# Kernel optimization log

Measured on AMD Instinct MI355X. Metric: run time of the kernel, lower is better.

Reference implementation:

```python
import jax, jax.numpy as jnp
import numpy as np

B, S, H, NH = 4, 2048, 1024, 16
HD = H // NH  # head dim 64


def setup_inputs() -> dict:
    key = jax.random.key(0)
    ks = jax.random.split(key, 8)
    s = 1.0 / np.sqrt(H)
    return {
        "hidden_states": jax.random.normal(ks[0], (B, S, H), dtype=jnp.float32),
        "attention_mask": jnp.zeros((B, 1, 1, S), dtype=jnp.float32),
        "Wq": jax.random.normal(ks[1], (H, H), dtype=jnp.float32) * s,
        "bq": jnp.zeros((H,), dtype=jnp.float32),
        "Wk": jax.random.normal(ks[2], (H, H), dtype=jnp.float32) * s,
        "bk": jnp.zeros((H,), dtype=jnp.float32),
        "Wv": jax.random.normal(ks[3], (H, H), dtype=jnp.float32) * s,
        "bv": jnp.zeros((H,), dtype=jnp.float32),
    }


def _split_heads(x):
    # [B,S,H] -> [B,NH,S,HD]
    b, s, _ = x.shape
    return x.reshape(b, s, NH, HD).transpose(0, 2, 1, 3)


def reference(hidden_states, attention_mask, Wq, bq, Wk, bk, Wv, bv):
    q = _split_heads(hidden_states @ Wq.T + bq)
    k = _split_heads(hidden_states @ Wk.T + bk)
    v = _split_heads(hidden_states @ Wv.T + bv)

    qk = jnp.einsum("bhid,bhjd->bhij", q, k)  # [B,NH,S,S]
    seq = q.shape[2]
    causal = jnp.triu(jnp.ones((seq, seq), dtype=bool), 1)  # True above diagonal
    attn_w = jnp.where(causal, -jnp.inf, qk) + attention_mask
    # NOTE: original divides by sqrt(d_k) AFTER masking/adding attention_mask
    probs = jax.nn.softmax(attn_w / jnp.sqrt(jnp.float32(HD)), axis=-1)
    out = jnp.einsum("bhij,bhjd->bhid", probs, v)  # [B,NH,S,HD]
    return out.transpose(0, 2, 1, 3).reshape(hidden_states.shape[0], seq, NH * HD)
```

## Files before the change

kernel.cpp:

```cpp
#include <hip/hip_runtime.h>


#define B_   4
#define S_   2048
#define H_   1024
#define NH_  16
#define HD_  64
#define M_   (B_ * S_)

#define CEXP 0.18033688011112042f

#define SWZ(row, col) ((col) ^ (((row) & 7) << 3))

typedef float          f32x4  __attribute__((ext_vector_type(4)));
typedef short          bf16x8 __attribute__((ext_vector_type(8)));
typedef unsigned short u16x8  __attribute__((ext_vector_type(8)));

__device__ __forceinline__ unsigned short f2bf(float f) {
    unsigned int u = __float_as_uint(f);
    u += 0x7fffu + ((u >> 16) & 1u);
    return (unsigned short)(u >> 16);
}

__device__ __forceinline__ void load16_lds(const unsigned short* g, unsigned short* l) {
    __builtin_amdgcn_global_load_lds(
        (const __attribute__((address_space(1))) unsigned int*)g,
        (__attribute__((address_space(3))) unsigned int*)l, 16, 0, 0);
}

__global__ __launch_bounds__(256) void cast_bf16(
    const float* __restrict__ s0, const float* __restrict__ s1,
    const float* __restrict__ s2, const float* __restrict__ s3,
    const float* __restrict__ s4,
    unsigned short* __restrict__ d0, unsigned short* __restrict__ d1,
    unsigned short* __restrict__ d2, unsigned short* __restrict__ d3,
    float* __restrict__ d4) {
    const int z = blockIdx.y;
    int i = (blockIdx.x * 256 + threadIdx.x) * 8;
    if (z == 4) {
        if (i + 8 <= B_ * S_) {
            float4 a = *(const float4*)(s4 + i);
            float4 b = *(const float4*)(s4 + i + 4);
            a.x *= CEXP; a.y *= CEXP; a.z *= CEXP; a.w *= CEXP;
            b.x *= CEXP; b.y *= CEXP; b.z *= CEXP; b.w *= CEXP;
            *(float4*)(d4 + i)     = a;
            *(float4*)(d4 + i + 4) = b;
        }
        return;
    }
    const float* src = (z == 0) ? s0 : (z == 1) ? s1 : (z == 2) ? s2 : s3;
    unsigned short* dst = (z == 0) ? d0 : (z == 1) ? d1 : (z == 2) ? d2 : d3;
    const int n = (z == 0) ? M_ * H_ : H_ * H_;
    if (i + 8 <= n) {
        float4 a = *(const float4*)(src + i);
        float4 b = *(const float4*)(src + i + 4);
        u16x8 o;
        o[0] = f2bf(a.x); o[1] = f2bf(a.y); o[2] = f2bf(a.z); o[3] = f2bf(a.w);
        o[4] = f2bf(b.x); o[5] = f2bf(b.y); o[6] = f2bf(b.z); o[7] = f2bf(b.w);
        *(u16x8*)(dst + i) = o;
    }
}

__global__ __launch_bounds__(256, 3) void qkv_gemm(
    const unsigned short* __restrict__ A,
    const unsigned short* __restrict__ W0, const unsigned short* __restrict__ W1,
    const unsigned short* __restrict__ W2,
    const float* __restrict__ b0, const float* __restrict__ b1,
    const float* __restrict__ b2,
    unsigned short* __restrict__ o0, unsigned short* __restrict__ o1,
    unsigned short* __restrict__ o2) {
    __shared__ unsigned short smem[2 * 128 * 64];
    unsigned short* sA = smem;
    unsigned short* sB = smem + 128 * 64;
    unsigned short* sT = smem;

    const int t = threadIdx.x;
    const int w = t >> 6, lane = t & 63, quad = lane >> 4, l15 = lane & 15;
    const int bm = blockIdx.x, bn = blockIdx.y, z = blockIdx.z;

    const unsigned short* W = (z == 0) ? W0 : (z == 1) ? W1 : W2;
    const float*        bia = (z == 0) ? b0 : (z == 1) ? b1 : b2;

    const int wm = (w & 1) * 64, wn = (w >> 1) * 64;

    f32x4 acc[4][4];
#pragma unroll
    for (int i = 0; i < 4; ++i)
#pragma unroll
        for (int j = 0; j < 4; ++j) acc[i][j] = f32x4{0.f, 0.f, 0.f, 0.f};

    const int srow = w * 32 + (lane >> 3);
    const int scol = (lane & 7) * 8;
    const unsigned short* Ag = A + (size_t)(bm * 128 + srow) * H_ + scol;
    const unsigned short* Wg = W + (size_t)(bn * 128 + srow) * H_ + scol;
    unsigned short* lA = &sA[w * 32 * 64];
    unsigned short* lB = &sB[w * 32 * 64];

    for (int kt = 0; kt < 16; ++kt) {
        __syncthreads();
#pragma unroll
        for (int c = 0; c < 4; ++c) {
            load16_lds(Ag + kt * 64 + (size_t)c * 8 * H_, lA + c * 512);
            load16_lds(Wg + kt * 64 + (size_t)c * 8 * H_, lB + c * 512);
        }
        __syncthreads();
#pragma unroll
        for (int kk = 0; kk < 64; kk += 32) {
            bf16x8 af[4], bf[4];
#pragma unroll
            for (int mi = 0; mi < 4; ++mi)
                af[mi] = *(const bf16x8*)&sA[(wm + mi * 16 + l15) * 64 + kk + quad * 8];
#pragma unroll
            for (int ni = 0; ni < 4; ++ni)
                bf[ni] = *(const bf16x8*)&sB[(wn + ni * 16 + l15) * 64 + kk + quad * 8];
#pragma unroll
            for (int mi = 0; mi < 4; ++mi)
#pragma unroll
                for (int ni = 0; ni < 4; ++ni)
                    acc[mi][ni] = __builtin_amdgcn_mfma_f32_16x16x32_bf16(
                        af[mi], bf[ni], acc[mi][ni], 0, 0, 0);
        }
    }

    float bvv[4];
#pragma unroll
    for (int ni = 0; ni < 4; ++ni) bvv[ni] = bia[bn * 128 + wn + ni * 16 + l15];

    if (z != 2) {
        unsigned short* outp = (z == 0) ? o0 : o1;
#pragma unroll
        for (int mi = 0; mi < 4; ++mi)
#pragma unroll
            for (int ni = 0; ni < 4; ++ni)
#pragma unroll
                for (int r = 0; r < 4; ++r) {
                    int m = bm * 128 + wm + mi * 16 + quad * 4 + r;
                    int n = bn * 128 + wn + ni * 16 + l15;
                    outp[(size_t)m * H_ + n] = f2bf(acc[mi][ni][r] + bvv[ni]);
                }
    } else {
        __syncthreads();
        const int halfw = w >> 1;
        const int bb = bm >> 4;
        const int s0 = (bm * 128) & 2047;
        for (int half = 0; half < 2; ++half) {
            if (half) __syncthreads();
            if (halfw == half) {
#pragma unroll
                for (int mi = 0; mi < 4; ++mi)
#pragma unroll
                    for (int ni = 0; ni < 4; ++ni)
#pragma unroll
                        for (int r = 0; r < 4; ++r) {
                            int nl = ni * 16 + l15;
                            int m  = wm + mi * 16 + quad * 4 + r;
                            sT[nl * 136 + m] = f2bf(acc[mi][ni][r] + bvv[ni]);
                        }
            }
            __syncthreads();
            {
                int nl = t >> 2, mc = (t & 3) * 32;
                int ng = bn * 128 + half * 64 + nl;
                int hh = ng >> 6, d = ng & 63;
                size_t base = ((size_t)((bb * NH_ + hh) * HD_ + d)) * S_ + s0 + mc;
#pragma unroll
                for (int i = 0; i < 4; ++i)
                    *(u16x8*)(o2 + base + i * 8) = *(const u16x8*)&sT[nl * 136 + mc + i * 8];
            }
        }
    }
}

__global__ __launch_bounds__(256, 3) void attn(
    const unsigned short* __restrict__ qg, const unsigned short* __restrict__ kg,
    const unsigned short* __restrict__ vtg, const float* __restrict__ mcg,
    float* __restrict__ outg) {
    __shared__ unsigned short k_s[2][64 * 64];
    __shared__ unsigned short v_s[2][64 * 64];
    __shared__ unsigned short p_s[4][16 * 64];

    const int t = threadIdx.x;
    const int w = t >> 6, lane = t & 63, quad = lane >> 4, l15 = lane & 15;
    const int lid = blockIdx.x;
    const int bh = (lid & 7) + ((lid >> 7) << 3);
    const int qt = (lid >> 3) & 15;
    const int b = bh >> 4, h = bh & 15;
    const int qa = qt, qb = 31 - qt;

    const int rs_ = t >> 2;
    const int cs_ = (t & 3) * 16;
    const int sc0 = rs_ * 64 + SWZ(rs_, cs_);
    const int sc1 = rs_ * 64 + SWZ(rs_, cs_ + 8);

    const unsigned short* kbase = kg + ((size_t)b * S_ + rs_) * H_ + h * HD_ + cs_;
    const unsigned short* vbase = vtg + ((size_t)bh * HD_ + rs_) * S_ + cs_;
    const float* mbase = mcg + b * S_ + l15;

    bf16x8 aqa[2], aqb[2];
    {
        const unsigned short* qpa =
            qg + ((size_t)(b * S_ + qa * 64 + w * 16 + l15)) * H_ + h * HD_ + quad * 8;
        aqa[0] = *(const bf16x8*)qpa;
        aqa[1] = *(const bf16x8*)(qpa + 32);
        const unsigned short* qpb =
            qg + ((size_t)(b * S_ + qb * 64 + w * 16 + l15)) * H_ + h * HD_ + quad * 8;
        aqb[0] = *(const bf16x8*)qpb;
        aqb[1] = *(const bf16x8*)(qpb + 32);
    }

    u16x8 pk0 = *(const u16x8*)kbase, pk1 = *(const u16x8*)(kbase + 8);
    u16x8 pv0 = *(const u16x8*)vbase, pv1 = *(const u16x8*)(vbase + 8);
    float pmc[4];
#pragma unroll
    for (int j = 0; j < 4; ++j) pmc[j] = mbase[j * 16];

    f32x4 oa[4], ob[4];
    float la[4] = {0.f, 0.f, 0.f, 0.f}, lb[4] = {0.f, 0.f, 0.f, 0.f};
#pragma unroll
    for (int dt = 0; dt < 4; ++dt) {
        oa[dt] = f32x4{0.f, 0.f, 0.f, 0.f};
        ob[dt] = f32x4{0.f, 0.f, 0.f, 0.f};
    }

    const int iga0 = qa * 64 + w * 16 + quad * 4;
    const int igb0 = qb * 64 + w * 16 + quad * 4;

    for (int kt = 0; kt <= qb; ++kt) {
        const int cur = kt & 1;
        *(u16x8*)&k_s[cur][sc0] = pk0;
        *(u16x8*)&k_s[cur][sc1] = pk1;
        *(u16x8*)&v_s[cur][sc0] = pv0;
        *(u16x8*)&v_s[cur][sc1] = pv1;
        float mc_[4];
#pragma unroll
        for (int j = 0; j < 4; ++j) mc_[j] = pmc[j];
        if (kt < qb) {
            const unsigned short* kp = kbase + (size_t)(kt + 1) * 64 * H_;
            pk0 = *(const u16x8*)kp; pk1 = *(const u16x8*)(kp + 8);
            const unsigned short* vp = vbase + (kt + 1) * 64;
            pv0 = *(const u16x8*)vp; pv1 = *(const u16x8*)(vp + 8);
#pragma unroll
            for (int j = 0; j < 4; ++j) pmc[j] = mbase[(kt + 1) * 64 + j * 16];
        }
        __syncthreads();

        {
            f32x4 sc[4];
#pragma unroll
            for (int jt = 0; jt < 4; ++jt) sc[jt] = f32x4{0.f, 0.f, 0.f, 0.f};
            __builtin_amdgcn_s_setprio(1);
#pragma unroll
            for (int c = 0; c < 2; ++c)
#pragma unroll
                for (int jt = 0; jt < 4; ++jt) {
                    int row = jt * 16 + l15;
                    bf16x8 bk = *(const bf16x8*)&k_s[cur][row * 64 + SWZ(row, c * 32 + quad * 8)];
                    sc[jt] = __builtin_amdgcn_mfma_f32_16x16x32_bf16(aqb[c], bk, sc[jt], 0, 0, 0);
                }
            __builtin_amdgcn_s_setprio(0);
            const bool diag = (kt == qb);
#pragma unroll
            for (int r = 0; r < 4; ++r) {
                float ls = 0.f;
                const int prow = quad * 4 + r;
#pragma unroll
                for (int jt = 0; jt < 4; ++jt) {
                    float p = __builtin_amdgcn_exp2f(__builtin_fmaf(sc[jt][r], CEXP, mc_[jt]));
                    if (diag && (kt * 64 + jt * 16 + l15) > (igb0 + r)) p = 0.f;
                    ls += p;
                    unsigned int u = __float_as_uint(p) + 0x8000u;
                    p_s[w][prow * 64 + SWZ(prow, jt * 16 + l15)] = (unsigned short)(u >> 16);
                }
                lb[r] += ls;
            }
            __builtin_amdgcn_s_setprio(1);
#pragma unroll
            for (int c = 0; c < 2; ++c) {
                bf16x8 ap = *(const bf16x8*)&p_s[w][l15 * 64 + SWZ(l15, c * 32 + quad * 8)];
#pragma unroll
                for (int dt = 0; dt < 4; ++dt) {
                    int row = dt * 16 + l15;
                    bf16x8 bv = *(const bf16x8*)&v_s[cur][row * 64 + SWZ(row, c * 32 + quad * 8)];
                    ob[dt] = __builtin_amdgcn_mfma_f32_16x16x32_bf16(ap, bv, ob[dt], 0, 0, 0);
                }
            }
            __builtin_amdgcn_s_setprio(0);
        }
        if (kt <= qa) {
            f32x4 sc[4];
#pragma unroll
            for (int jt = 0; jt < 4; ++jt) sc[jt] = f32x4{0.f, 0.f, 0.f, 0.f};
            __builtin_amdgcn_s_setprio(1);
#pragma unroll
            for (int c = 0; c < 2; ++c)
#pragma unroll
                for (int jt = 0; jt < 4; ++jt) {
                    int row = jt * 16 + l15;
                    bf16x8 bk = *(const bf16x8*)&k_s[cur][row * 64 + SWZ(row, c * 32 + quad * 8)];
                    sc[jt] = __builtin_amdgcn_mfma_f32_16x16x32_bf16(aqa[c], bk, sc[jt], 0, 0, 0);
                }
            __builtin_amdgcn_s_setprio(0);
            const bool diag = (kt == qa);
#pragma unroll
            for (int r = 0; r < 4; ++r) {
                float ls = 0.f;
                const int prow = quad * 4 + r;
#pragma unroll
                for (int jt = 0; jt < 4; ++jt) {
                    float p = __builtin_amdgcn_exp2f(__builtin_fmaf(sc[jt][r], CEXP, mc_[jt]));
                    if (diag && (kt * 64 + jt * 16 + l15) > (iga0 + r)) p = 0.f;
                    ls += p;
                    unsigned int u = __float_as_uint(p) + 0x8000u;
                    p_s[w][prow * 64 + SWZ(prow, jt * 16 + l15)] = (unsigned short)(u >> 16);
                }
                la[r] += ls;
            }
            __builtin_amdgcn_s_setprio(1);
#pragma unroll
            for (int c = 0; c < 2; ++c) {
                bf16x8 ap = *(const bf16x8*)&p_s[w][l15 * 64 + SWZ(l15, c * 32 + quad * 8)];
#pragma unroll
                for (int dt = 0; dt < 4; ++dt) {
                    int row = dt * 16 + l15;
                    bf16x8 bv = *(const bf16x8*)&v_s[cur][row * 64 + SWZ(row, c * 32 + quad * 8)];
                    oa[dt] = __builtin_amdgcn_mfma_f32_16x16x32_bf16(ap, bv, oa[dt], 0, 0, 0);
                }
            }
            __builtin_amdgcn_s_setprio(0);
        }
    }

#pragma unroll
    for (int r = 0; r < 4; ++r) {
        float sa = la[r], sb = lb[r];
#pragma unroll
        for (int mk = 1; mk <= 8; mk <<= 1) {
            sa += __shfl_xor(sa, mk);
            sb += __shfl_xor(sb, mk);
        }
        la[r] = 1.0f / sa;
        lb[r] = 1.0f / sb;
    }
#pragma unroll
    for (int dt = 0; dt < 4; ++dt)
#pragma unroll
        for (int r = 0; r < 4; ++r) {
            int col = h * HD_ + dt * 16 + l15;
            outg[(size_t)(b * S_ + iga0 + r) * H_ + col] = oa[dt][r] * la[r];
            outg[(size_t)(b * S_ + igb0 + r) * H_ + col] = ob[dt][r] * lb[r];
        }
}

extern "C" void kernel_launch(void* const* d_in, const int* in_sizes, int n_in,
                              void* d_out, int out_size, void* d_ws, size_t ws_size,
                              hipStream_t stream) {
    const float* hs   = (const float*)d_in[0];
    const float* mask = (const float*)d_in[1];
    const float* Wq   = (const float*)d_in[2];
    const float* bq   = (const float*)d_in[3];
    const float* Wk   = (const float*)d_in[4];
    const float* bk   = (const float*)d_in[5];
    const float* Wv   = (const float*)d_in[6];
    const float* bv   = (const float*)d_in[7];
    float* out = (float*)d_out;

    unsigned short* hsb = (unsigned short*)d_ws;
    unsigned short* wqb = hsb + (size_t)M_ * H_;
    unsigned short* wkb = wqb + (size_t)H_ * H_;
    unsigned short* wvb = wkb + (size_t)H_ * H_;
    unsigned short* qb  = wvb + (size_t)H_ * H_;
    unsigned short* kb  = qb  + (size_t)M_ * H_;
    unsigned short* vtb = kb  + (size_t)M_ * H_;
    float*          mcw = (float*)(vtb + (size_t)M_ * H_);

    cast_bf16<<<dim3((M_ * H_) / 2048, 5), 256, 0, stream>>>(
        hs, Wq, Wk, Wv, mask, hsb, wqb, wkb, wvb, mcw);

    qkv_gemm<<<dim3(M_ / 128, H_ / 128, 3), 256, 0, stream>>>(
        hsb, wqb, wkb, wvb, bq, bk, bv, qb, kb, vtb);

    attn<<<dim3(1024), 256, 0, stream>>>(qb, kb, vtb, mcw, out);
}
```

Baseline: 235.1 us.

## Interleave both query tiles' QK and PV MFMAs to share K/V fragment loads

Both query tiles (qa and qb) now run their QK^T MFMAs unconditionally in one loop that shares each K fragment read from LDS. Each tile writes its probabilities to its own LDS buffer, and the PV MFMAs are likewise interleaved so every V fragment is read once for both tiles. This halves K/V LDS reads and gives the MFMA pipe two independent accumulation chains to overlap. The cost is wasted MFMA work for tile qa on iterations past its causal range (it multiplies zeroed probabilities), extra LDS for the second P buffer, and higher register pressure that may hurt occupancy at 3 blocks per SM.

```diff
diff --git a/kernel.cpp b/kernel.cpp
--- a/kernel.cpp
+++ b/kernel.cpp
@@ -177,7 +177,8 @@
     float* __restrict__ outg) {
     __shared__ unsigned short k_s[2][64 * 64];
     __shared__ unsigned short v_s[2][64 * 64];
-    __shared__ unsigned short p_s[4][16 * 64];
+    __shared__ unsigned short pa_s[4][16 * 64];
+    __shared__ unsigned short pb_s[4][16 * 64];
 
     const int t = threadIdx.x;
     const int w = t >> 6, lane = t & 63, quad = lane >> 4, l15 = lane & 15;
@@ -244,20 +245,27 @@
         }
         __syncthreads();
 
+        const bool runa = (kt <= qa);
+
+        f32x4 sca[4], scb[4];
+#pragma unroll
+        for (int jt = 0; jt < 4; ++jt) {
+            sca[jt] = f32x4{0.f, 0.f, 0.f, 0.f};
+            scb[jt] = f32x4{0.f, 0.f, 0.f, 0.f};
+        }
+        __builtin_amdgcn_s_setprio(1);
+#pragma unroll
+        for (int c = 0; c < 2; ++c)
+#pragma unroll
+            for (int jt = 0; jt < 4; ++jt) {
+                int row = jt * 16 + l15;
+                bf16x8 bk = *(const bf16x8*)&k_s[cur][row * 64 + SWZ(row, c * 32 + quad * 8)];
+                scb[jt] = __builtin_amdgcn_mfma_f32_16x16x32_bf16(aqb[c], bk, scb[jt], 0, 0, 0);
+                sca[jt] = __builtin_amdgcn_mfma_f32_16x16x32_bf16(aqa[c], bk, sca[jt], 0, 0, 0);
+            }
+        __builtin_amdgcn_s_setprio(0);
+
         {
-            f32x4 sc[4];
-#pragma unroll
-            for (int jt = 0; jt < 4; ++jt) sc[jt] = f32x4{0.f, 0.f, 0.f, 0.f};
-            __builtin_amdgcn_s_setprio(1);
-#pragma unroll
-            for (int c = 0; c < 2; ++c)
-#pragma unroll
-                for (int jt = 0; jt < 4; ++jt) {
-                    int row = jt * 16 + l15;
-                    bf16x8 bk = *(const bf16x8*)&k_s[cur][row * 64 + SWZ(row, c * 32 + quad * 8)];
-                    sc[jt] = __builtin_amdgcn_mfma_f32_16x16x32_bf16(aqb[c], bk, sc[jt], 0, 0, 0);
-                }
-            __builtin_amdgcn_s_setprio(0);
             const bool diag = (kt == qb);
 #pragma unroll
             for (int r = 0; r < 4; ++r) {
@@ -265,41 +273,16 @@
                 const int prow = quad * 4 + r;
 #pragma unroll
                 for (int jt = 0; jt < 4; ++jt) {
-                    float p = __builtin_amdgcn_exp2f(__builtin_fmaf(sc[jt][r], CEXP, mc_[jt]));
+                    float p = __builtin_amdgcn_exp2f(__builtin_fmaf(scb[jt][r], CEXP, mc_[jt]));
                     if (diag && (kt * 64 + jt * 16 + l15) > (igb0 + r)) p = 0.f;
                     ls += p;
                     unsigned int u = __float_as_uint(p) + 0x8000u;
-                    p_s[w][prow * 64 + SWZ(prow, jt * 16 + l15)] = (unsigned short)(u >> 16);
+                    pb_s[w][prow * 64 + SWZ(prow, jt * 16 + l15)] = (unsigned short)(u >> 16);
                 }
                 lb[r] += ls;
             }
-            __builtin_amdgcn_s_setprio(1);
-#pragma unroll
-            for (int c = 0; c < 2; ++c) {
-                bf16x8 ap = *(const bf16x8*)&p_s[w][l15 * 64 + SWZ(l15, c * 32 + quad * 8)];
-#pragma unroll
-                for (int dt = 0; dt < 4; ++dt) {
-                    int row = dt * 16 + l15;
-                    bf16x8 bv = *(const bf16x8*)&v_s[cur][row * 64 + SWZ(row, c * 32 + quad * 8)];
-                    ob[dt] = __builtin_amdgcn_mfma_f32_16x16x32_bf16(ap, bv, ob[dt], 0, 0, 0);
-                }
-            }
-            __builtin_amdgcn_s_setprio(0);
-        }
-        if (kt <= qa) {
-            f32x4 sc[4];
-#pragma unroll
-            for (int jt = 0; jt < 4; ++jt) sc[jt] = f32x4{0.f, 0.f, 0.f, 0.f};
-            __builtin_amdgcn_s_setprio(1);
-#pragma unroll
-            for (int c = 0; c < 2; ++c)
-#pragma unroll
-                for (int jt = 0; jt < 4; ++jt) {
-                    int row = jt * 16 + l15;
-                    bf16x8 bk = *(const bf16x8*)&k_s[cur][row * 64 + SWZ(row, c * 32 + quad * 8)];
-                    sc[jt] = __builtin_amdgcn_mfma_f32_16x16x32_bf16(aqa[c], bk, sc[jt], 0, 0, 0);
-                }
-            __builtin_amdgcn_s_setprio(0);
+        }
+        if (runa) {
             const bool diag = (kt == qa);
 #pragma unroll
             for (int r = 0; r < 4; ++r) {
@@ -307,27 +290,31 @@
                 const int prow = quad * 4 + r;
 #pragma unroll
                 for (int jt = 0; jt < 4; ++jt) {
-                    float p = __builtin_amdgcn_exp2f(__builtin_fmaf(sc[jt][r], CEXP, mc_[jt]));
+                    float p = __builtin_amdgcn_exp2f(__builtin_fmaf(sca[jt][r], CEXP, mc_[jt]));
                     if (diag && (kt * 64 + jt * 16 + l15) > (iga0 + r)) p = 0.f;
                     ls += p;
                     unsigned int u = __float_as_uint(p) + 0x8000u;
-                    p_s[w][prow * 64 + SWZ(prow, jt * 16 + l15)] = (unsigned short)(u >> 16);
+                    pa_s[w][prow * 64 + SWZ(prow, jt * 16 + l15)] = (unsigned short)(u >> 16);
                 }
                 la[r] += ls;
             }
-            __builtin_amdgcn_s_setprio(1);
-#pragma unroll
-            for (int c = 0; c < 2; ++c) {
-                bf16x8 ap = *(const bf16x8*)&p_s[w][l15 * 64 + SWZ(l15, c * 32 + quad * 8)];
-#pragma unroll
-                for (int dt = 0; dt < 4; ++dt) {
-                    int row = dt * 16 + l15;
-                    bf16x8 bv = *(const bf16x8*)&v_s[cur][row * 64 + SWZ(row, c * 32 + quad * 8)];
-                    oa[dt] = __builtin_amdgcn_mfma_f32_16x16x32_bf16(ap, bv, oa[dt], 0, 0, 0);
-                }
-            }
-            __builtin_amdgcn_s_setprio(0);
-        }
+        }
+
+        __builtin_amdgcn_s_setprio(1);
+#pragma unroll
+        for (int c = 0; c < 2; ++c) {
+            bf16x8 apb = *(const bf16x8*)&pb_s[w][l15 * 64 + SWZ(l15, c * 32 + quad * 8)];
+            bf16x8 apa = *(const bf16x8*)&pa_s[w][l15 * 64 + SWZ(l15, c * 32 + quad * 8)];
+            if (!runa) apa = bf16x8{0, 0, 0, 0, 0, 0, 0, 0};
+#pragma unroll
+            for (int dt = 0; dt < 4; ++dt) {
+                int row = dt * 16 + l15;
+                bf16x8 bv = *(const bf16x8*)&v_s[cur][row * 64 + SWZ(row, c * 32 + quad * 8)];
+                ob[dt] = __builtin_amdgcn_mfma_f32_16x16x32_bf16(apb, bv, ob[dt], 0, 0, 0);
+                oa[dt] = __builtin_amdgcn_mfma_f32_16x16x32_bf16(apa, bv, oa[dt], 0, 0, 0);
+            }
+        }
+        __builtin_amdgcn_s_setprio(0);
     }
 
 #pragma unroll
```

Result: slower. 251.1 us (+6.8%).

## Transpose QK MFMA operands, pack softmax probs with cvt_pk_bf16, compact cast grid

Applied to the files above, without the earlier changes.

The attention kernel swaps the QK^T MFMA operands so each lane holds four consecutive key columns for one query row. That lets it read the mask as float4 vectors, convert pairs of probabilities with v_cvt_pk_bf16_f32, and write 8-byte packed stores to LDS instead of scalar 16-bit stores. The row-sum reduction becomes a per-lane scalar plus two cross-quad shuffles, redistributed at the end. The cast kernel is flattened into a 1D grid sized exactly to the work, which removes idle blocks from the old 5x4096 grid; the mask loads now happen after the barrier instead of being prefetched.

```diff
diff --git a/kernel.cpp b/kernel.cpp
--- a/kernel.cpp
+++ b/kernel.cpp
@@ -15,11 +15,18 @@
 typedef float          f32x4  __attribute__((ext_vector_type(4)));
 typedef short          bf16x8 __attribute__((ext_vector_type(8)));
 typedef unsigned short u16x8  __attribute__((ext_vector_type(8)));
+typedef unsigned int   u32x2  __attribute__((ext_vector_type(2)));
 
 __device__ __forceinline__ unsigned short f2bf(float f) {
     unsigned int u = __float_as_uint(f);
     u += 0x7fffu + ((u >> 16) & 1u);
     return (unsigned short)(u >> 16);
+}
+
+__device__ __forceinline__ unsigned int cvt_pk_bf16(float lo, float hi) {
+    unsigned int r;
+    asm("v_cvt_pk_bf16_f32 %0, %1, %2" : "=v"(r) : "v"(lo), "v"(hi));
+    return r;
 }
 
 __device__ __forceinline__ void load16_lds(const unsigned short* g, unsigned short* l) {
@@ -35,9 +42,9 @@
     unsigned short* __restrict__ d0, unsigned short* __restrict__ d1,
     unsigned short* __restrict__ d2, unsigned short* __restrict__ d3,
     float* __restrict__ d4) {
-    const int z = blockIdx.y;
-    int i = (blockIdx.x * 256 + threadIdx.x) * 8;
-    if (z == 4) {
+    const int bid = blockIdx.x;
+    if (bid >= 5632) {
+        int i = ((bid - 5632) * 256 + (int)threadIdx.x) * 8;
         if (i + 8 <= B_ * S_) {
             float4 a = *(const float4*)(s4 + i);
             float4 b = *(const float4*)(s4 + i + 4);
@@ -48,17 +55,20 @@
         }
         return;
     }
-    const float* src = (z == 0) ? s0 : (z == 1) ? s1 : (z == 2) ? s2 : s3;
-    unsigned short* dst = (z == 0) ? d0 : (z == 1) ? d1 : (z == 2) ? d2 : d3;
-    const int n = (z == 0) ? M_ * H_ : H_ * H_;
-    if (i + 8 <= n) {
-        float4 a = *(const float4*)(src + i);
-        float4 b = *(const float4*)(src + i + 4);
-        u16x8 o;
-        o[0] = f2bf(a.x); o[1] = f2bf(a.y); o[2] = f2bf(a.z); o[3] = f2bf(a.w);
-        o[4] = f2bf(b.x); o[5] = f2bf(b.y); o[6] = f2bf(b.z); o[7] = f2bf(b.w);
-        *(u16x8*)(dst + i) = o;
-    }
+    const float* src;
+    unsigned short* dst;
+    int base;
+    if (bid < 4096)      { src = s0; dst = d0; base = bid; }
+    else if (bid < 4608) { src = s1; dst = d1; base = bid - 4096; }
+    else if (bid < 5120) { src = s2; dst = d2; base = bid - 4608; }
+    else                 { src = s3; dst = d3; base = bid - 5120; }
+    int i = (base * 256 + (int)threadIdx.x) * 8;
+    float4 a = *(const float4*)(src + i);
+    float4 b = *(const float4*)(src + i + 4);
+    u16x8 o;
+    o[0] = f2bf(a.x); o[1] = f2bf(a.y); o[2] = f2bf(a.z); o[3] = f2bf(a.w);
+    o[4] = f2bf(b.x); o[5] = f2bf(b.y); o[6] = f2bf(b.z); o[7] = f2bf(b.w);
+    *(u16x8*)(dst + i) = o;
 }
 
 __global__ __launch_bounds__(256, 3) void qkv_gemm(
@@ -194,7 +204,7 @@
 
     const unsigned short* kbase = kg + ((size_t)b * S_ + rs_) * H_ + h * HD_ + cs_;
     const unsigned short* vbase = vtg + ((size_t)bh * HD_ + rs_) * S_ + cs_;
-    const float* mbase = mcg + b * S_ + l15;
+    const float* mrow = mcg + b * S_ + quad * 4;
 
     bf16x8 aqa[2], aqb[2];
     {
@@ -210,20 +220,20 @@
 
     u16x8 pk0 = *(const u16x8*)kbase, pk1 = *(const u16x8*)(kbase + 8);
     u16x8 pv0 = *(const u16x8*)vbase, pv1 = *(const u16x8*)(vbase + 8);
-    float pmc[4];
-#pragma unroll
-    for (int j = 0; j < 4; ++j) pmc[j] = mbase[j * 16];
 
     f32x4 oa[4], ob[4];
-    float la[4] = {0.f, 0.f, 0.f, 0.f}, lb[4] = {0.f, 0.f, 0.f, 0.f};
+    float lsa = 0.f, lsb = 0.f;
 #pragma unroll
     for (int dt = 0; dt < 4; ++dt) {
         oa[dt] = f32x4{0.f, 0.f, 0.f, 0.f};
         ob[dt] = f32x4{0.f, 0.f, 0.f, 0.f};
     }
 
-    const int iga0 = qa * 64 + w * 16 + quad * 4;
-    const int igb0 = qb * 64 + w * 16 + quad * 4;
+    const int iga0  = qa * 64 + w * 16 + quad * 4;
+    const int igb0  = qb * 64 + w * 16 + quad * 4;
+    const int qcola = qa * 64 + w * 16 + l15;
+    const int qcolb = qb * 64 + w * 16 + l15;
+    const int pwr0 = l15 * 64;
 
     for (int kt = 0; kt <= qb; ++kt) {
         const int cur = kt & 1;
@@ -231,18 +241,18 @@
         *(u16x8*)&k_s[cur][sc1] = pk1;
         *(u16x8*)&v_s[cur][sc0] = pv0;
         *(u16x8*)&v_s[cur][sc1] = pv1;
-        float mc_[4];
-#pragma unroll
-        for (int j = 0; j < 4; ++j) mc_[j] = pmc[j];
         if (kt < qb) {
             const unsigned short* kp = kbase + (size_t)(kt + 1) * 64 * H_;
             pk0 = *(const u16x8*)kp; pk1 = *(const u16x8*)(kp + 8);
             const unsigned short* vp = vbase + (kt + 1) * 64;
             pv0 = *(const u16x8*)vp; pv1 = *(const u16x8*)(vp + 8);
-#pragma unroll
-            for (int j = 0; j < 4; ++j) pmc[j] = mbase[(kt + 1) * 64 + j * 16];
         }
         __syncthreads();
+
+        float4 mcv[4];
+#pragma unroll
+        for (int jt = 0; jt < 4; ++jt)
+            mcv[jt] = *(const float4*)(mrow + kt * 64 + jt * 16);
 
         {
             f32x4 sc[4];
@@ -255,23 +265,28 @@
                 for (int jt = 0; jt < 4; ++jt) {
                     int row = jt * 16 + l15;
                     bf16x8 bk = *(const bf16x8*)&k_s[cur][row * 64 + SWZ(row, c * 32 + quad * 8)];
-                    sc[jt] = __builtin_amdgcn_mfma_f32_16x16x32_bf16(aqb[c], bk, sc[jt], 0, 0, 0);
+                    sc[jt] = __builtin_amdgcn_mfma_f32_16x16x32_bf16(bk, aqb[c], sc[jt], 0, 0, 0);
                 }
             __builtin_amdgcn_s_setprio(0);
             const bool diag = (kt == qb);
 #pragma unroll
-            for (int r = 0; r < 4; ++r) {
-                float ls = 0.f;
-                const int prow = quad * 4 + r;
-#pragma unroll
-                for (int jt = 0; jt < 4; ++jt) {
-                    float p = __builtin_amdgcn_exp2f(__builtin_fmaf(sc[jt][r], CEXP, mc_[jt]));
-                    if (diag && (kt * 64 + jt * 16 + l15) > (igb0 + r)) p = 0.f;
-                    ls += p;
-                    unsigned int u = __float_as_uint(p) + 0x8000u;
-                    p_s[w][prow * 64 + SWZ(prow, jt * 16 + l15)] = (unsigned short)(u >> 16);
-                }
-                lb[r] += ls;
+            for (int jt = 0; jt < 4; ++jt) {
+                const int sb0 = kt * 64 + jt * 16 + quad * 4;
+                float p0 = __builtin_amdgcn_exp2f(__builtin_fmaf(sc[jt][0], CEXP, mcv[jt].x));
+                float p1 = __builtin_amdgcn_exp2f(__builtin_fmaf(sc[jt][1], CEXP, mcv[jt].y));
+                float p2 = __builtin_amdgcn_exp2f(__builtin_fmaf(sc[jt][2], CEXP, mcv[jt].z));
+                float p3 = __builtin_amdgcn_exp2f(__builtin_fmaf(sc[jt][3], CEXP, mcv[jt].w));
+                if (diag) {
+                    if (sb0 + 0 > qcolb) p0 = 0.f;
+                    if (sb0 + 1 > qcolb) p1 = 0.f;
+                    if (sb0 + 2 > qcolb) p2 = 0.f;
+                    if (sb0 + 3 > qcolb) p3 = 0.f;
+                }
+                lsb += (p0 + p1) + (p2 + p3);
+                u32x2 pw;
+                pw[0] = cvt_pk_bf16(p0, p1);
+                pw[1] = cvt_pk_bf16(p2, p3);
+                *(u32x2*)&p_s[w][pwr0 + SWZ(l15, jt * 16 + quad * 4)] = pw;
             }
             __builtin_amdgcn_s_setprio(1);
 #pragma unroll
@@ -297,23 +312,28 @@
                 for (int jt = 0; jt < 4; ++jt) {
                     int row = jt * 16 + l15;
                     bf16x8 bk = *(const bf16x8*)&k_s[cur][row * 64 + SWZ(row, c * 32 + quad * 8)];
-                    sc[jt] = __builtin_amdgcn_mfma_f32_16x16x32_bf16(aqa[c], bk, sc[jt], 0, 0, 0);
+                    sc[jt] = __builtin_amdgcn_mfma_f32_16x16x32_bf16(bk, aqa[c], sc[jt], 0, 0, 0);
                 }
             __builtin_amdgcn_s_setprio(0);
             const bool diag = (kt == qa);
 #pragma unroll
-            for (int r = 0; r < 4; ++r) {
-                float ls = 0.f;
-                const int prow = quad * 4 + r;
-#pragma unroll
-                for (int jt = 0; jt < 4; ++jt) {
-                    float p = __builtin_amdgcn_exp2f(__builtin_fmaf(sc[jt][r], CEXP, mc_[jt]));
-                    if (diag && (kt * 64 + jt * 16 + l15) > (iga0 + r)) p = 0.f;
-                    ls += p;
-                    unsigned int u = __float_as_uint(p) + 0x8000u;
-                    p_s[w][prow * 64 + SWZ(prow, jt * 16 + l15)] = (unsigned short)(u >> 16);
-                }
-                la[r] += ls;
+            for (int jt = 0; jt < 4; ++jt) {
+                const int sb0 = kt * 64 + jt * 16 + quad * 4;
+                float p0 = __builtin_amdgcn_exp2f(__builtin_fmaf(sc[jt][0], CEXP, mcv[jt].x));
+                float p1 = __builtin_amdgcn_exp2f(__builtin_fmaf(sc[jt][1], CEXP, mcv[jt].y));
+                float p2 = __builtin_amdgcn_exp2f(__builtin_fmaf(sc[jt][2], CEXP, mcv[jt].z));
+                float p3 = __builtin_amdgcn_exp2f(__builtin_fmaf(sc[jt][3], CEXP, mcv[jt].w));
+                if (diag) {
+                    if (sb0 + 0 > qcola) p0 = 0.f;
+                    if (sb0 + 1 > qcola) p1 = 0.f;
+                    if (sb0 + 2 > qcola) p2 = 0.f;
+                    if (sb0 + 3 > qcola) p3 = 0.f;
+                }
+                lsa += (p0 + p1) + (p2 + p3);
+                u32x2 pw;
+                pw[0] = cvt_pk_bf16(p0, p1);
+                pw[1] = cvt_pk_bf16(p2, p3);
+                *(u32x2*)&p_s[w][pwr0 + SWZ(l15, jt * 16 + quad * 4)] = pw;
             }
             __builtin_amdgcn_s_setprio(1);
 #pragma unroll
@@ -330,24 +350,23 @@
         }
     }
 
+    float sa = lsa, sb = lsb;
+    sa += __shfl_xor(sa, 16); sa += __shfl_xor(sa, 32);
+    sb += __shfl_xor(sb, 16); sb += __shfl_xor(sb, 32);
+    float ra[4], rb[4];
 #pragma unroll
     for (int r = 0; r < 4; ++r) {
-        float sa = la[r], sb = lb[r];
-#pragma unroll
-        for (int mk = 1; mk <= 8; mk <<= 1) {
-            sa += __shfl_xor(sa, mk);
-            sb += __shfl_xor(sb, mk);
-        }
-        la[r] = 1.0f / sa;
-        lb[r] = 1.0f / sb;
+        int src = (quad << 4) | (quad * 4 + r);
+        ra[r] = 1.0f / __shfl(sa, src);
+        rb[r] = 1.0f / __shfl(sb, src);
     }
 #pragma unroll
     for (int dt = 0; dt < 4; ++dt)
 #pragma unroll
         for (int r = 0; r < 4; ++r) {
             int col = h * HD_ + dt * 16 + l15;
-            outg[(size_t)(b * S_ + iga0 + r) * H_ + col] = oa[dt][r] * la[r];
-            outg[(size_t)(b * S_ + igb0 + r) * H_ + col] = ob[dt][r] * lb[r];
+            outg[(size_t)(b * S_ + iga0 + r) * H_ + col] = oa[dt][r] * ra[r];
+            outg[(size_t)(b * S_ + igb0 + r) * H_ + col] = ob[dt][r] * rb[r];
         }
 }
 
@@ -373,7 +392,7 @@
     unsigned short* vtb = kb  + (size_t)M_ * H_;
     float*          mcw = (float*)(vtb + (size_t)M_ * H_);
 
-    cast_bf16<<<dim3((M_ * H_) / 2048, 5), 256, 0, stream>>>(
+    cast_bf16<<<dim3(5636), 256, 0, stream>>>(
         hs, Wq, Wk, Wv, mask, hsb, wqb, wkb, wvb, mcw);
 
     qkv_gemm<<<dim3(M_ / 128, H_ / 128, 3), 256, 0, stream>>>(
```

Result: faster. 228.7 us (-2.7%).
